# Kernel tuning notes

Hardware: AMD Instinct MI355X
Metric: run time of the kernel (lower is better)

The kernel has to match this reference:

```python
import jax, jax.numpy as jnp
import numpy as np

NEG_SLOPE = 0.2

def leaky_relu(x):
    return jnp.where(x >= 0, x, NEG_SLOPE * x)

def conv1x1(x, w, b):
    # x: [n,c,h,w], w: [o,c], b: [o]
    return jnp.einsum('nchw,oc->nohw', x, w) + b[None, :, None, None]

def setup_inputs() -> dict:
    key = jax.random.key(0)
    ks = jax.random.split(key, 7)
    n, c, h, w = 4, 64, 80, 80
    scale = 1.0 / np.sqrt(c)
    return {
        'x': jax.random.normal(ks[0], (n, c, h, w), dtype=jnp.float32),
        'w1': jax.random.normal(ks[1], (c, c), dtype=jnp.float32) * scale,
        'b1': jax.random.normal(ks[2], (c,), dtype=jnp.float32) * 0.01,
        'w2': jax.random.normal(ks[3], (c, c), dtype=jnp.float32) * scale,
        'b2': jax.random.normal(ks[4], (c,), dtype=jnp.float32) * 0.01,
        'w3': jax.random.normal(ks[5], (c, c), dtype=jnp.float32) * scale,
        'b3': jax.random.normal(ks[6], (c,), dtype=jnp.float32) * 0.01,
    }

def reference(x, w1, b1, w2, b2, w3, b3):
    n, c, h, w = x.shape
    e1 = leaky_relu(conv1x1(x, w1, b1))  # [n,c,h,w]
    e2 = leaky_relu(conv1x1(x, w2, b2))
    asm = leaky_relu(conv1x1(x, w3, b3))
    # q: [n, hw, c]; k: [n, c, hw]
    q = e1.transpose(0, 2, 3, 1).reshape(n, h * w, c)
    k = e2.reshape(n, c, h * w)
    score = jax.nn.softmax(jnp.matmul(q, k), axis=2)  # [n, hw, hw]
    v = asm.reshape(n, c, h * w).transpose(0, 2, 1)   # [n, hw, c]
    out = jnp.matmul(score, v)                        # [n, hw, c]
    return out.transpose(0, 2, 1).reshape(n, c, h, w)
```

## Files before the change

kernel.cpp:

```cpp
#include <hip/hip_runtime.h>


typedef __attribute__((ext_vector_type(8))) unsigned short us8;
typedef __attribute__((ext_vector_type(4))) unsigned short us4;
typedef __attribute__((ext_vector_type(8))) __bf16 bf16x8;
typedef __attribute__((ext_vector_type(16))) float f32x16;

#define HW 6400
#define L2E 1.44269504088896340736f
#define SHIFT 32.0f
#define KS 5
#define ITERS 20

union V8 { us8 s; us4 h[2]; bf16x8 b; unsigned u4[4]; };

__device__ __forceinline__ unsigned short f32_to_bf16(float f) {
  unsigned u = __float_as_uint(f);
  u += 0x7fffu + ((u >> 16) & 1u);
  return (unsigned short)(u >> 16);
}
__device__ __forceinline__ float bf16_bits_to_f32(unsigned short u) {
  return __uint_as_float(((unsigned)u) << 16);
}
__device__ __forceinline__ unsigned pack_bf16x2(float a, float b) {
#if __has_builtin(__builtin_amdgcn_cvt_pk_bf16_f32)
  auto v = __builtin_amdgcn_cvt_pk_bf16_f32(a, b);
  unsigned u;
  __builtin_memcpy(&u, &v, 4);
  return u;
#else
  unsigned ua = __float_as_uint(a); ua += 0x7fffu + ((ua >> 16) & 1u);
  unsigned ub = __float_as_uint(b); ub += 0x7fffu + ((ub >> 16) & 1u);
  return (ua >> 16) | (ub & 0xffff0000u);
#endif
}

__device__ __forceinline__ void split_hilo(const float* f, V8& hi, V8& lo) {
#pragma unroll
  for (int j = 0; j < 8; ++j) {
    const unsigned short h = f32_to_bf16(f[j]);
    const float r = f[j] - bf16_bits_to_f32(h);
    hi.s[j] = h;
    lo.s[j] = f32_to_bf16(r);
  }
}

__global__ __launch_bounds__(256, 2) void conv_kernel(
    const float* __restrict__ x,
    const float* __restrict__ w1, const float* __restrict__ b1,
    const float* __restrict__ w2, const float* __restrict__ b2,
    const float* __restrict__ w3, const float* __restrict__ b3,
    unsigned short* __restrict__ Qg, unsigned short* __restrict__ Kg,
    unsigned short* __restrict__ Vg) {
  __shared__ __align__(16) float xs[64 * 132];
  __shared__ __align__(16) unsigned short tb[128 * 72];

  const int t = threadIdx.x;
  const int n = blockIdx.y;
  const int p0 = blockIdx.x * 128;
  const int wv = t >> 6;
  const int lane = t & 63;
  const int l31 = lane & 31;
  const int lh = lane >> 5;
  const int ob = (wv & 1) * 32;
  const int pw = (wv >> 1) * 64;

  {
    const int c = t >> 2, qq = t & 3;
    const float* src = x + ((size_t)(n * 64 + c) * HW + p0 + qq * 32);
    float* dst = xs + c * 132 + qq * 32;
#pragma unroll
    for (int i = 0; i < 8; ++i)
      *(float4*)(dst + i * 4) = *(const float4*)(src + i * 4);
  }
  __syncthreads();

  const float* wms[3] = {w1, w2, w3};
  const float* bms[3] = {b1, b2, b3};

#pragma unroll 1
  for (int k = 0; k < 3; ++k) {
    const float* wm = wms[k];
    const float* bm = bms[k];

    V8 ah[4], al[4];
#pragma unroll
    for (int kst = 0; kst < 4; ++kst) {
      const float* wr = wm + (size_t)(ob + l31) * 64 + kst * 16 + lh * 8;
      float wf[8];
      *(float4*)(wf) = *(const float4*)wr;
      *(float4*)(wf + 4) = *(const float4*)(wr + 4);
      split_hilo(wf, ah[kst], al[kst]);
    }

    f32x16 acc[2];
#pragma unroll
    for (int pb = 0; pb < 2; ++pb)
#pragma unroll
      for (int r = 0; r < 16; ++r) acc[pb][r] = 0.f;

#pragma unroll
    for (int kst = 0; kst < 4; ++kst) {
#pragma unroll
      for (int pb = 0; pb < 2; ++pb) {
        float xf[8];
        const float* xp = xs + (kst * 16 + lh * 8) * 132 + pw + pb * 32 + l31;
#pragma unroll
        for (int j = 0; j < 8; ++j) xf[j] = xp[j * 132];
        V8 bh, bl;
        split_hilo(xf, bh, bl);
        acc[pb] = __builtin_amdgcn_mfma_f32_32x32x16_bf16(al[kst].b, bh.b, acc[pb], 0, 0, 0);
        acc[pb] = __builtin_amdgcn_mfma_f32_32x32x16_bf16(ah[kst].b, bl.b, acc[pb], 0, 0, 0);
        acc[pb] = __builtin_amdgcn_mfma_f32_32x32x16_bf16(ah[kst].b, bh.b, acc[pb], 0, 0, 0);
      }
    }

    if (k < 2) {
#pragma unroll
      for (int pb = 0; pb < 2; ++pb) {
#pragma unroll
        for (int rq = 0; rq < 4; ++rq) {
          const int o = ob + 8 * rq + 4 * lh;
          const int pcol = pw + pb * 32 + l31;
          float v[4];
#pragma unroll
          for (int j = 0; j < 4; ++j) {
            float a = acc[pb][4 * rq + j] + bm[o + j];
            a = fmaxf(a, 0.f) + 0.2f * fminf(a, 0.f);
            if (k == 0) a *= L2E;
            v[j] = a;
          }
          unsigned* dst = (unsigned*)(tb + pcol * 72 + o);
          dst[0] = pack_bf16x2(v[0], v[1]);
          dst[1] = pack_bf16x2(v[2], v[3]);
        }
      }
      __syncthreads();
      {
        const int p = t >> 1, half = t & 1;
        const unsigned short* src = tb + p * 72 + half * 32;
        unsigned short* dst = (k == 0 ? Qg : Kg) +
                              (size_t)(n * HW + p0 + p) * 64 + half * 32;
#pragma unroll
        for (int i = 0; i < 4; ++i) *(us8*)(dst + i * 8) = *(const us8*)(src + i * 8);
      }
      __syncthreads();
    } else {
#pragma unroll
      for (int pb = 0; pb < 2; ++pb) {
#pragma unroll
        for (int r = 0; r < 16; ++r) {
          const int o = ob + 8 * (r >> 2) + 4 * lh + (r & 3);
          const int pcol = pw + pb * 32 + l31;
          float a = acc[pb][r] + bm[o];
          a = fmaxf(a, 0.f) + 0.2f * fminf(a, 0.f);
          Vg[(size_t)(n * 64 + o) * HW + p0 + pcol] = f32_to_bf16(a);
        }
      }
    }
  }
}

__global__ __launch_bounds__(256, 2) void attn_kernel(
    const unsigned short* __restrict__ Qg, const unsigned short* __restrict__ Kg,
    const unsigned short* __restrict__ Vg, float* __restrict__ Opart,
    float* __restrict__ Lpart) {
  __shared__ __align__(16) char smem[36864];
  float* Ot = (float*)smem;

  const int t = threadIdx.x;
  const int w = t >> 6;
  const int lane = t & 63;
  const int l31 = lane & 31;
  const int lh = lane >> 5;
  const int nb = blockIdx.y;
  const int qb = blockIdx.x * 256;
  const int ks = blockIdx.z;
  const int key0 = ks * (HW / KS);

  V8 aQ[2][4];
#pragma unroll
  for (int qh = 0; qh < 2; ++qh) {
    const unsigned short* qrow =
        Qg + (size_t)(nb * HW + qb + w * 64 + qh * 32 + l31) * 64 + lh * 8;
#pragma unroll
    for (int kst = 0; kst < 4; ++kst) aQ[qh][kst].s = *(const us8*)(qrow + kst * 16);
  }

  f32x16 accO[2][2];
#pragma unroll
  for (int qh = 0; qh < 2; ++qh)
#pragma unroll
    for (int ci = 0; ci < 2; ++ci)
#pragma unroll
      for (int r = 0; r < 16; ++r) accO[qh][ci][r] = 0.f;
  float lp[2] = {0.f, 0.f};

  const int soff = (t >> 2) * 72 + (t & 3) * 16;
  const unsigned short* ksrc =
      Kg + (size_t)nb * HW * 64 + (size_t)(key0 + (t >> 2)) * 64 + (t & 3) * 16;
  const unsigned short* vsrc =
      Vg + (size_t)nb * 64 * HW + (size_t)(t >> 2) * HW + key0 + (t & 3) * 16;

  V8 kr0, kr1, vr0, vr1;
  kr0.s = *(const us8*)ksrc;
  kr1.s = *(const us8*)(ksrc + 8);
  vr0.s = *(const us8*)vsrc;
  vr1.s = *(const us8*)(vsrc + 8);
  {
    unsigned short* kd = (unsigned short*)smem + soff;
    unsigned short* vd = (unsigned short*)(smem + 18432) + soff;
    *(us8*)kd = kr0.s; *(us8*)(kd + 8) = kr1.s;
    *(us8*)vd = vr0.s; *(us8*)(vd + 8) = vr1.s;
  }
  __syncthreads();

#pragma unroll 1
  for (int jt = 0; jt < ITERS; ++jt) {
    const int b = jt & 1;
    const unsigned short* Kc = (const unsigned short*)(smem + b * 9216);
    const unsigned short* Vc = (const unsigned short*)(smem + 18432 + b * 9216);
    const bool more = (jt + 1 < ITERS);

    if (more) {
      kr0.s = *(const us8*)(ksrc + (jt + 1) * 4096);
      kr1.s = *(const us8*)(ksrc + (jt + 1) * 4096 + 8);
      vr0.s = *(const us8*)(vsrc + (jt + 1) * 64);
      vr1.s = *(const us8*)(vsrc + (jt + 1) * 64 + 8);
    }

    V8 ak[2][4];
#pragma unroll
    for (int ni = 0; ni < 2; ++ni)
#pragma unroll
      for (int kst = 0; kst < 4; ++kst)
        ak[ni][kst].s = *(const us8*)(Kc + (ni * 32 + l31) * 72 + kst * 16 + lh * 8);

    uint2 pkq[2][2][4];
#pragma unroll
    for (int qh = 0; qh < 2; ++qh) {
#pragma unroll
      for (int ni = 0; ni < 2; ++ni) {
        f32x16 sacc;
#pragma unroll
        for (int r = 0; r < 16; ++r) sacc[r] = 0.f;
#pragma unroll
        for (int kst = 0; kst < 4; ++kst)
          sacc = __builtin_amdgcn_mfma_f32_32x32x16_bf16(ak[ni][kst].b,
                                                         aQ[qh][kst].b, sacc, 0, 0, 0);
#pragma unroll
        for (int g = 0; g < 4; ++g) {
          const float p0 = __builtin_amdgcn_exp2f(sacc[4 * g + 0] - SHIFT);
          const float p1 = __builtin_amdgcn_exp2f(sacc[4 * g + 1] - SHIFT);
          const float p2 = __builtin_amdgcn_exp2f(sacc[4 * g + 2] - SHIFT);
          const float p3 = __builtin_amdgcn_exp2f(sacc[4 * g + 3] - SHIFT);
          lp[qh] += (p0 + p1) + (p2 + p3);
          pkq[qh][ni][g].x = pack_bf16x2(p0, p1);
          pkq[qh][ni][g].y = pack_bf16x2(p2, p3);
        }
      }
    }

    V8 bv[2][4];
#pragma unroll
    for (int ci = 0; ci < 2; ++ci)
#pragma unroll
      for (int kst = 0; kst < 4; ++kst)
        bv[ci][kst].s = *(const us8*)(Vc + (ci * 32 + l31) * 72 + kst * 16 + lh * 8);

#pragma unroll
    for (int qh = 0; qh < 2; ++qh) {
#pragma unroll
      for (int kst = 0; kst < 4; ++kst) {
        const int ni = kst >> 1;
        const int gb = 2 * (kst & 1);
        const uint2 qa = pkq[qh][ni][gb];
        const uint2 qb2 = pkq[qh][ni][gb + 1];
        uint2 send;
        send.x = lh ? qa.x : qb2.x;
        send.y = lh ? qa.y : qb2.y;
        uint2 recv;
        recv.x = __shfl_xor(send.x, 32);
        recv.y = __shfl_xor(send.y, 32);
        const uint2 keep = {lh ? qb2.x : qa.x, lh ? qb2.y : qa.y};
        V8 ap;
        ap.u4[0] = lh ? recv.x : keep.x;
        ap.u4[1] = lh ? recv.y : keep.y;
        ap.u4[2] = lh ? keep.x : recv.x;
        ap.u4[3] = lh ? keep.y : recv.y;
        accO[qh][0] = __builtin_amdgcn_mfma_f32_32x32x16_bf16(ap.b, bv[0][kst].b,
                                                              accO[qh][0], 0, 0, 0);
        accO[qh][1] = __builtin_amdgcn_mfma_f32_32x32x16_bf16(ap.b, bv[1][kst].b,
                                                              accO[qh][1], 0, 0, 0);
      }
    }

    if (more) {
      unsigned short* kd = (unsigned short*)(smem + (1 - b) * 9216) + soff;
      unsigned short* vd = (unsigned short*)(smem + 18432 + (1 - b) * 9216) + soff;
      *(us8*)kd = kr0.s; *(us8*)(kd + 8) = kr1.s;
      *(us8*)vd = vr0.s; *(us8*)(vd + 8) = vr1.s;
      __syncthreads();
    }
  }

#pragma unroll
  for (int qh = 0; qh < 2; ++qh) {
    const float lsum = lp[qh] + __shfl_xor(lp[qh], 32);
    if (lh == 0)
      Lpart[((size_t)ks * 4 + nb) * HW + qb + w * 64 + qh * 32 + l31] = lsum;
  }

#pragma unroll 1
  for (int pi = 0; pi < 2; ++pi) {
    __syncthreads();
    if ((w >> 1) == pi) {
#pragma unroll
      for (int qh = 0; qh < 2; ++qh)
#pragma unroll
        for (int ci = 0; ci < 2; ++ci)
#pragma unroll
          for (int r = 0; r < 16; ++r) {
            const int qcol = (w & 1) * 64 + qh * 32 + 8 * (r >> 2) + 4 * lh + (r & 3);
            Ot[(ci * 32 + l31) * 132 + qcol] = accO[qh][ci][r];
          }
    }
    __syncthreads();
    {
      const int ch = t >> 2, part = t & 3;
      const float* src = Ot + ch * 132 + part * 32;
      float* dst = Opart + ((size_t)ks * 4 + nb) * (64 * HW) + (size_t)ch * HW +
                   qb + pi * 128 + part * 32;
#pragma unroll
      for (int i = 0; i < 8; ++i)
        *(float4*)(dst + i * 4) = *(const float4*)(src + i * 4);
    }
  }
}

__global__ __launch_bounds__(256) void combine_kernel(
    const float* __restrict__ Opart, const float* __restrict__ Lpart,
    float* __restrict__ out) {
  const int tid = blockIdx.x * 256 + threadIdx.x;
  const size_t e = (size_t)tid * 4;
  float4 o = {0.f, 0.f, 0.f, 0.f};
#pragma unroll
  for (int ks = 0; ks < KS; ++ks) {
    const float4 v = *(const float4*)(Opart + (size_t)ks * (4 * 64 * HW) + e);
    o.x += v.x; o.y += v.y; o.z += v.z; o.w += v.w;
  }
  const int n = (int)(e / (64 * HW));
  const int p = (int)(e % HW);
  float4 l = {0.f, 0.f, 0.f, 0.f};
#pragma unroll
  for (int ks = 0; ks < KS; ++ks) {
    const float4 v = *(const float4*)(Lpart + ((size_t)ks * 4 + n) * HW + p);
    l.x += v.x; l.y += v.y; l.z += v.z; l.w += v.w;
  }
  float4 r;
  r.x = o.x / l.x; r.y = o.y / l.y; r.z = o.z / l.z; r.w = o.w / l.w;
  *(float4*)(out + e) = r;
}

extern "C" void kernel_launch(void* const* d_in, const int* in_sizes, int n_in,
                              void* d_out, int out_size, void* d_ws, size_t ws_size,
                              hipStream_t stream) {
  const float* x = (const float*)d_in[0];
  const float* w1 = (const float*)d_in[1];
  const float* b1 = (const float*)d_in[2];
  const float* w2 = (const float*)d_in[3];
  const float* b2 = (const float*)d_in[4];
  const float* w3 = (const float*)d_in[5];
  const float* b3 = (const float*)d_in[6];
  float* out = (float*)d_out;

  unsigned short* Q = (unsigned short*)d_ws;
  unsigned short* K = Q + (size_t)4 * HW * 64;
  unsigned short* V = K + (size_t)4 * HW * 64;
  float* Opart = (float*)(V + (size_t)4 * HW * 64);
  float* Lpart = Opart + (size_t)KS * 4 * 64 * HW;

  conv_kernel<<<dim3(50, 4), 256, 0, stream>>>(x, w1, b1, w2, b2, w3, b3,
                                               Q, K, V);
  attn_kernel<<<dim3(25, 4, KS), 256, 0, stream>>>(Q, K, V, Opart, Lpart);
  combine_kernel<<<1600, 256, 0, stream>>>(Opart, Lpart, out);
}
```

Before: 154.3 us.

## Double key splits, store attention partials in bf16, fold exp shift into MFMA init

Raises the number of key-dimension splits from 5 to 10 (halving iterations per block) so the attention launch has twice as many blocks to fill the GPU. Partial output accumulators are now written to workspace as bf16 instead of fp32, halving partial-write and combine-read traffic that would otherwise double with more splits. The constant softmax shift is folded into the MFMA accumulator initial value, removing a subtraction per score. Costs include more combine work and bf16 rounding of partial sums before reduction.

After: 155.5 us. No clear change (+0.8%).

```diff
diff --git a/kernel.cpp b/kernel.cpp
--- a/kernel.cpp
+++ b/kernel.cpp
@@ -9,8 +9,8 @@
 #define HW 6400
 #define L2E 1.44269504088896340736f
 #define SHIFT 32.0f
-#define KS 5
-#define ITERS 20
+#define KS 10
+#define ITERS 10
 
 union V8 { us8 s; us4 h[2]; bf16x8 b; unsigned u4[4]; };
 
@@ -163,10 +163,10 @@
 
 __global__ __launch_bounds__(256, 2) void attn_kernel(
     const unsigned short* __restrict__ Qg, const unsigned short* __restrict__ Kg,
-    const unsigned short* __restrict__ Vg, float* __restrict__ Opart,
+    const unsigned short* __restrict__ Vg, unsigned short* __restrict__ Opart,
     float* __restrict__ Lpart) {
   __shared__ __align__(16) char smem[36864];
-  float* Ot = (float*)smem;
+  unsigned short* Otb = (unsigned short*)smem;
 
   const int t = threadIdx.x;
   const int w = t >> 6;
@@ -243,17 +243,17 @@
       for (int ni = 0; ni < 2; ++ni) {
         f32x16 sacc;
 #pragma unroll
-        for (int r = 0; r < 16; ++r) sacc[r] = 0.f;
+        for (int r = 0; r < 16; ++r) sacc[r] = -SHIFT;
 #pragma unroll
         for (int kst = 0; kst < 4; ++kst)
           sacc = __builtin_amdgcn_mfma_f32_32x32x16_bf16(ak[ni][kst].b,
                                                          aQ[qh][kst].b, sacc, 0, 0, 0);
 #pragma unroll
         for (int g = 0; g < 4; ++g) {
-          const float p0 = __builtin_amdgcn_exp2f(sacc[4 * g + 0] - SHIFT);
-          const float p1 = __builtin_amdgcn_exp2f(sacc[4 * g + 1] - SHIFT);
-          const float p2 = __builtin_amdgcn_exp2f(sacc[4 * g + 2] - SHIFT);
-          const float p3 = __builtin_amdgcn_exp2f(sacc[4 * g + 3] - SHIFT);
+          const float p0 = __builtin_amdgcn_exp2f(sacc[4 * g + 0]);
+          const float p1 = __builtin_amdgcn_exp2f(sacc[4 * g + 1]);
+          const float p2 = __builtin_amdgcn_exp2f(sacc[4 * g + 2]);
+          const float p3 = __builtin_amdgcn_exp2f(sacc[4 * g + 3]);
           lp[qh] += (p0 + p1) + (p2 + p3);
           pkq[qh][ni][g].x = pack_bf16x2(p0, p1);
           pkq[qh][ni][g].y = pack_bf16x2(p2, p3);
@@ -322,32 +322,39 @@
 #pragma unroll
           for (int r = 0; r < 16; ++r) {
             const int qcol = (w & 1) * 64 + qh * 32 + 8 * (r >> 2) + 4 * lh + (r & 3);
-            Ot[(ci * 32 + l31) * 132 + qcol] = accO[qh][ci][r];
+            Otb[(ci * 32 + l31) * 132 + qcol] = f32_to_bf16(accO[qh][ci][r]);
           }
     }
     __syncthreads();
     {
       const int ch = t >> 2, part = t & 3;
-      const float* src = Ot + ch * 132 + part * 32;
-      float* dst = Opart + ((size_t)ks * 4 + nb) * (64 * HW) + (size_t)ch * HW +
-                   qb + pi * 128 + part * 32;
-#pragma unroll
-      for (int i = 0; i < 8; ++i)
-        *(float4*)(dst + i * 4) = *(const float4*)(src + i * 4);
+      const unsigned short* src = Otb + ch * 132 + part * 32;
+      unsigned short* dst = Opart + (((size_t)ks * 4 + nb) * 64 + ch) * HW +
+                            qb + pi * 128 + part * 32;
+#pragma unroll
+      for (int i = 0; i < 4; ++i) {
+        V8 v;
+        v.h[0] = *(const us4*)(src + i * 8);
+        v.h[1] = *(const us4*)(src + i * 8 + 4);
+        *(us8*)(dst + i * 8) = v.s;
+      }
     }
   }
 }
 
 __global__ __launch_bounds__(256) void combine_kernel(
-    const float* __restrict__ Opart, const float* __restrict__ Lpart,
+    const unsigned short* __restrict__ Opart, const float* __restrict__ Lpart,
     float* __restrict__ out) {
   const int tid = blockIdx.x * 256 + threadIdx.x;
   const size_t e = (size_t)tid * 4;
   float4 o = {0.f, 0.f, 0.f, 0.f};
 #pragma unroll
   for (int ks = 0; ks < KS; ++ks) {
-    const float4 v = *(const float4*)(Opart + (size_t)ks * (4 * 64 * HW) + e);
-    o.x += v.x; o.y += v.y; o.z += v.z; o.w += v.w;
+    const us4 v = *(const us4*)(Opart + (size_t)ks * (4 * 64 * HW) + e);
+    o.x += bf16_bits_to_f32(v[0]);
+    o.y += bf16_bits_to_f32(v[1]);
+    o.z += bf16_bits_to_f32(v[2]);
+    o.w += bf16_bits_to_f32(v[3]);
   }
   const int n = (int)(e / (64 * HW));
   const int p = (int)(e % HW);
@@ -377,8 +384,8 @@
   unsigned short* Q = (unsigned short*)d_ws;
   unsigned short* K = Q + (size_t)4 * HW * 64;
   unsigned short* V = K + (size_t)4 * HW * 64;
-  float* Opart = (float*)(V + (size_t)4 * HW * 64);
-  float* Lpart = Opart + (size_t)KS * 4 * 64 * HW;
+  unsigned short* Opart = V + (size_t)4 * HW * 64;
+  float* Lpart = (float*)(Opart + (size_t)KS * 4 * 64 * HW);
 
   conv_kernel<<<dim3(50, 4), 256, 0, stream>>>(x, w1, b1, w2, b2, w3, b3,
                                                Q, K, V);
```
